# Optimization experiments

Measured on AMD Instinct MI355X. Metric: run time of the kernel, lower is better.

The kernel has to match this reference:

```python
import jax, jax.numpy as jnp
import numpy as np

B, T, C = 2, 2048, 2048
N_HEAD, D_HEAD = 16, 128

def setup_inputs() -> dict:
    key = jax.random.key(0)
    k1, k2, k3 = jax.random.split(key, 3)
    x = jax.random.normal(k1, (B, T, C), dtype=jnp.float32)
    # lecun-normal-ish scaling for kernels
    W_attn = jax.random.normal(k2, (C, 3 * C), dtype=jnp.float32) * (1.0 / np.sqrt(C))
    W_proj = jax.random.normal(k3, (C, C), dtype=jnp.float32) * (1.0 / np.sqrt(C))
    return {"x": x, "W_attn": W_attn, "W_proj": W_proj}

def reference(x, W_attn, W_proj):
    Bx, Tx, Cx = x.shape
    # fused qkv projection: (B,T,C) @ (C,3C)
    qkv = x @ W_attn
    q, k, v = jnp.split(qkv, 3, axis=-1)
    # (B, H, T, Dh)
    q = q.reshape(Bx, Tx, N_HEAD, D_HEAD).transpose(0, 2, 1, 3)
    k = k.reshape(Bx, Tx, N_HEAD, D_HEAD).transpose(0, 2, 1, 3)
    v = v.reshape(Bx, Tx, N_HEAD, D_HEAD).transpose(0, 2, 1, 3)
    scale = 1.0 / jnp.sqrt(jnp.asarray(D_HEAD, dtype=x.dtype))
    att = jnp.einsum('bhqd,bhkd->bhqk', q, k) * scale  # (B,H,T,T)
    causal_mask = jnp.tril(jnp.ones((Tx, Tx), dtype=jnp.bool_))[None, None]
    att = jnp.where(causal_mask, att, -jnp.inf)
    att = jax.nn.softmax(att, axis=-1)
    y = jnp.einsum('bhqk,bhkd->bhqd', att, v)
    y = y.transpose(0, 2, 1, 3).reshape(Bx, Tx, Cx)
    return y @ W_proj
```

## Files before the change

### kernel.cpp

```cpp
#include <hip/hip_runtime.h>
#include <hip/hip_bf16.h>
#include <stdint.h>

#define AS1 __attribute__((address_space(1)))
#define AS3 __attribute__((address_space(3)))

typedef __bf16 bf16_t;
typedef __bf16 bf16x8 __attribute__((ext_vector_type(8)));
typedef float f32x4 __attribute__((ext_vector_type(4)));
typedef float f32x16 __attribute__((ext_vector_type(16)));

static constexpr int Bsz = 2, T = 2048, Cdim = 2048, NH = 16, DH = 128;
static constexpr int M  = Bsz * T;
static constexpr int N1 = 3 * Cdim;
static constexpr int K1 = Cdim;

__device__ __forceinline__ unsigned short f2bf(float f) {
  unsigned u = __float_as_uint(f);
  u += 0x7fffu + ((u >> 16) & 1u);
  return (unsigned short)(u >> 16);
}

__device__ __forceinline__ void gload_lds16(const bf16_t* g, void* l) {
  __builtin_amdgcn_global_load_lds((AS1 const void*)g, (AS3 void*)l, 16, 0, 0);
}

__device__ __forceinline__ float ex2(float x) {
  float r; asm("v_exp_f32 %0, %1" : "=v"(r) : "v"(x)); return r;
}
__device__ __forceinline__ unsigned pk2(float a, float b) {
  unsigned r; asm("v_cvt_pk_bf16_f32 %0, %1, %2" : "=v"(r) : "v"(a), "v"(b)); return r;
}

__global__ __launch_bounds__(256) void preamble_kernel(const float* __restrict__ x,
                                                       const float* __restrict__ Wa,
                                                       const float* __restrict__ Wp,
                                                       unsigned short* __restrict__ xb,
                                                       unsigned short* __restrict__ WaT,
                                                       unsigned short* __restrict__ WpT) {
  __shared__ float tile[32][33];
  const int blk = blockIdx.x;
  const int tid = threadIdx.x;
  if (blk < 8192) {
    int i = blk * 1024 + tid * 4;
    float4 v = *(const float4*)(x + i);
    ushort4 o;
    o.x = f2bf(v.x); o.y = f2bf(v.y); o.z = f2bf(v.z); o.w = f2bf(v.w);
    *(ushort4*)(xb + i) = o;
    return;
  }
  const float* in;
  unsigned short* out;
  int Nn, bi;
  if (blk < 20480) { in = Wa; out = WaT; Nn = N1;   bi = blk - 8192;  }
  else             { in = Wp; out = WpT; Nn = Cdim; bi = blk - 20480; }
  const int ntiles = Nn >> 5;
  const int n0 = (bi % ntiles) * 32, k0 = (bi / ntiles) * 32;
  const int tx = tid & 31, ty = tid >> 5;
#pragma unroll
  for (int i = 0; i < 32; i += 8)
    tile[ty + i][tx] = in[(size_t)(k0 + ty + i) * Nn + n0 + tx];
  __syncthreads();
#pragma unroll
  for (int i = 0; i < 32; i += 8)
    out[(size_t)(n0 + ty + i) * K1 + k0 + tx] = f2bf(tile[tx][ty + i]);
}

template <int MODE>
__global__ __launch_bounds__(512, 4) void gemm_p3(const bf16_t* __restrict__ A,
                                                  const bf16_t* __restrict__ BT,
                                                  void* __restrict__ Cp,
                                                  int Nn, int Kk) {
  constexpr int SLOT = 24576;
  __shared__ __align__(16) char ldsmem[3 * SLOT];
  char* ldsb = ldsmem;

  const int tid = threadIdx.x;
  const int wid = tid >> 6, lane = tid & 63;
  const int lq = lane & 15, lk = lane >> 4;
  const int wr = wid >> 2, wc = wid & 3;

  const int bid = blockIdx.x;
  const int xcd = bid & 7;
  const int j = bid >> 3;
  const int r = j & 31, s5 = j >> 5;
  const int tn = s5 * 8 + (r & 7);
  const int tm = xcd * 4 + (r >> 3);

  f32x4 acc[4][4] = {};

  int aoff[4], boff[4];
#pragma unroll
  for (int m = 0; m < 4; ++m) {
    int row = wr * 64 + m * 16 + lq;
    aoff[m] = row * 64 + ((lk * 16) ^ (((row >> 1) & 3) << 4));
  }
#pragma unroll
  for (int n = 0; n < 4; ++n) {
    int brow = wc * 64 + n * 16 + lq;
    boff[n] = 8192 + brow * 64 + ((lk * 16) ^ (((brow >> 1) & 3) << 4));
  }

  const int pA = wid * 1024 + lane * 16;
  const int arow = pA >> 6;
  const int acsw = (pA & 63) ^ (((arow >> 1) & 3) << 4);
  const bf16_t* Ags = A + (size_t)(tm * 128 + arow) * Kk + (acsw >> 1);

  const int pB0 = wid * 1024 + lane * 16;
  const int brow0 = pB0 >> 6;
  const int bcsw0 = (pB0 & 63) ^ (((brow0 >> 1) & 3) << 4);
  const bf16_t* Bgs0 = BT + (size_t)(tn * 256 + brow0) * Kk + (bcsw0 >> 1);

  const int pB1 = 8192 + wid * 1024 + lane * 16;
  const int brow1 = pB1 >> 6;
  const int bcsw1 = (pB1 & 63) ^ (((brow1 >> 1) & 3) << 4);
  const bf16_t* Bgs1 = BT + (size_t)(tn * 256 + brow1) * Kk + (bcsw1 >> 1);

  const int ldsA = wid * 1024;
  const int ldsB0 = 8192 + wid * 1024;
  const int ldsB1 = 16384 + wid * 1024;

  auto stage = [&](int kt, int slot) {
    char* db = ldsb + slot * SLOT;
    gload_lds16(Ags + (size_t)kt * 32, db + ldsA);
    gload_lds16(Bgs0 + (size_t)kt * 32, db + ldsB0);
    gload_lds16(Bgs1 + (size_t)kt * 32, db + ldsB1);
  };

  const int nk = Kk >> 5;

  stage(0, 0); stage(1, 1);
  asm volatile("s_waitcnt vmcnt(3)" ::: "memory");
  __builtin_amdgcn_s_barrier();

#define TILE_BODY(KT, SLOT0, SLOT2, STAGE_EN, VM)                                \
  {                                                                              \
    __builtin_amdgcn_sched_barrier(0);                                           \
    const char* sb = ldsb + (SLOT0) * SLOT;                                      \
    bf16x8 af[4], bfv[4];                                                        \
    _Pragma("unroll") for (int m = 0; m < 4; ++m)                                \
      af[m] = *(const bf16x8*)(sb + aoff[m]);                                    \
    _Pragma("unroll") for (int n = 0; n < 4; ++n)                                \
      bfv[n] = *(const bf16x8*)(sb + boff[n]);                                   \
    if (STAGE_EN) stage((KT) + 2, (SLOT2));                                      \
    __builtin_amdgcn_sched_barrier(0);                                           \
    __builtin_amdgcn_s_barrier();                                                \
    asm volatile("s_waitcnt lgkmcnt(0)" ::: "memory");                           \
    __builtin_amdgcn_sched_barrier(0);                                           \
    __builtin_amdgcn_s_setprio(1);                                               \
    _Pragma("unroll") for (int m = 0; m < 4; ++m)                                \
      _Pragma("unroll") for (int n = 0; n < 4; ++n)                              \
        acc[m][n] =                                                              \
            __builtin_amdgcn_mfma_f32_16x16x32_bf16(af[m], bfv[n], acc[m][n], 0, 0, 0); \
    __builtin_amdgcn_s_setprio(0);                                               \
    __builtin_amdgcn_sched_barrier(0);                                           \
    asm volatile("s_waitcnt vmcnt(" #VM ")" ::: "memory");                       \
    __builtin_amdgcn_s_barrier();                                                \
  }

  {
    int c0 = 0;
    for (int kt = 0; kt < nk - 2; ++kt) {
      const int c2 = (c0 >= 1) ? (c0 - 1) : (c0 + 2);
      TILE_BODY(kt, c0, c2, 1, 3);
      c0 = (c0 >= 2) ? 0 : (c0 + 1);
    }
    TILE_BODY(nk - 2, c0, 0, 0, 0);
    c0 = (c0 >= 2) ? 0 : (c0 + 1);
    TILE_BODY(nk - 1, c0, 0, 0, 0);
  }
#undef TILE_BODY

  if (MODE == 1 && tn >= 16) {
    unsigned short* q16 = (unsigned short*)Cp;
#pragma unroll
    for (int m = 0; m < 4; ++m)
#pragma unroll
      for (int n = 0; n < 4; ++n) {
        int row = tm * 128 + wr * 64 + m * 16 + lk * 4;
        int b_ = row >> 11, t0 = row & 2047;
        int c = tn * 256 - 4096 + wc * 64 + n * 16 + lq;
        ushort4 o;
        o.x = f2bf(acc[m][n][0]); o.y = f2bf(acc[m][n][1]);
        o.z = f2bf(acc[m][n][2]); o.w = f2bf(acc[m][n][3]);
        *(ushort4*)(q16 + (size_t)(b_ * 2048 + c) * N1 + 4096 + t0) = o;
      }
  } else {
#pragma unroll
    for (int m = 0; m < 4; ++m)
#pragma unroll
      for (int n = 0; n < 4; ++n)
#pragma unroll
        for (int r2 = 0; r2 < 4; ++r2) {
          int row = tm * 128 + wr * 64 + m * 16 + lk * 4 + r2;
          int col = tn * 256 + wc * 64 + n * 16 + lq;
          if (MODE == 1)
            ((unsigned short*)Cp)[(size_t)row * Nn + col] = f2bf(acc[m][n][r2]);
          else
            ((float*)Cp)[(size_t)row * Nn + col] = acc[m][n][r2];
        }
  }
}

__global__ __launch_bounds__(512, 1) void attn_kernel(const bf16_t* __restrict__ qkv,
                                                      unsigned short* __restrict__ y) {
  __shared__ __align__(16) char lds[98304];
  const int tid = threadIdx.x;
  const int wid = tid >> 6, lane = tid & 63;
  const int l31 = lane & 31, hi = lane >> 5;
  const int hi16 = hi << 4;
  const int bh = blockIdx.x;
  const int g = blockIdx.y;
  const int b = bh >> 4, h = bh & 15;
  const float SC2 = 0.12751879868954096f;

  const int grp = (wid < 4) ? g : (15 - g);
  const int qlo = grp * 128 + (wid & 3) * 32;
  const int qidx = qlo + l31;
  const int nt = 2 * (15 - g) + 2;
  const size_t rowbase = (size_t)(b * T) * N1;

  bf16x8 qf[8];
  {
    const bf16_t* Qg = qkv + rowbase + (size_t)qidx * N1 + h * DH + hi * 8;
#pragma unroll
    for (int kk = 0; kk < 8; ++kk) qf[kk] = *(const bf16x8*)(Qg + kk * 16);
  }

  const bf16_t* Kg0 = qkv + rowbase + Cdim + h * DH;
  const bf16_t* Vg0 = qkv + (size_t)(b * 2048 + h * DH) * N1 + 2 * Cdim;
  const int p0 = wid * 1024 + lane * 16;
  const int p1 = 8192 + wid * 1024 + lane * 16;
  const int kr0 = p0 >> 8, kr1 = p1 >> 8;
  const bf16_t* KsA = Kg0 + (size_t)kr0 * N1 + ((((p0 & 255) ^ ((kr0 & 15) << 4))) >> 1);
  const bf16_t* KsB = Kg0 + (size_t)kr1 * N1 + ((((p1 & 255) ^ ((kr1 & 15) << 4))) >> 1);
  const int vr0 = p0 >> 7, vr1 = p1 >> 7;
  const bf16_t* VsA = Vg0 + (size_t)vr0 * N1 + ((((p0 & 127) ^ ((vr0 & 7) << 4))) >> 1);
  const bf16_t* VsB = Vg0 + (size_t)vr1 * N1 + ((((p1 & 127) ^ ((vr1 & 7) << 4))) >> 1);
  const int dstoff = wid * 1024;

  auto stage = [&](int tt, int slot) {
    char* Kd = lds + slot * 32768;
    char* Vd = Kd + 16384;
    const size_t ko = (size_t)(tt * 64) * N1;
    const int vo = tt * 64;
    gload_lds16(KsA + ko, Kd + dstoff);
    gload_lds16(KsB + ko, Kd + 8192 + dstoff);
    gload_lds16(VsA + vo, Vd + dstoff);
    gload_lds16(VsB + vo, Vd + 8192 + dstoff);
  };

  f32x16 oacc[4] = {};
  float mrow = -1e30f, lrow = 0.f;

  stage(0, 0); stage(1, 1);
  asm volatile("s_waitcnt vmcnt(4)" ::: "memory");
  __builtin_amdgcn_s_barrier();

  int cs = 0;
  for (int t = 0; t < nt; ++t) {
    const int kv0 = t * 64;
    if (t + 2 < nt) {
      const int s2 = (cs >= 1) ? (cs - 1) : (cs + 2);
      stage(t + 2, s2);
    }

    if (kv0 <= qlo + 31) {
      f32x16 s0 = {}, s1 = {};
      {
        const char* Kb = lds + cs * 32768;
        const char* krow0 = Kb + l31 * 256;
        const char* krow1 = Kb + (32 + l31) * 256;
        const int sw0 = (l31 & 15) << 4;
#pragma unroll
        for (int kk = 0; kk < 8; ++kk) {
          bf16x8 kf0 = *(const bf16x8*)(krow0 + ((kk * 32 + hi16) ^ sw0));
          bf16x8 kf1 = *(const bf16x8*)(krow1 + ((kk * 32 + hi16) ^ sw0));
          s0 = __builtin_amdgcn_mfma_f32_32x32x16_bf16(kf0, qf[kk], s0, 0, 0, 0);
          s1 = __builtin_amdgcn_mfma_f32_32x32x16_bf16(kf1, qf[kk], s1, 0, 0, 0);
        }
      }
      float sv[32];
#pragma unroll
      for (int r = 0; r < 16; ++r) { sv[r] = s0[r]; sv[16 + r] = s1[r]; }
      if (kv0 + 63 > qlo) {
#pragma unroll
        for (int r = 0; r < 16; ++r) {
          const int roff = (r & 3) + 8 * (r >> 2);
          if (kv0 + roff + 4 * hi > qidx) sv[r] = -1e30f;
          if (kv0 + 32 + roff + 4 * hi > qidx) sv[16 + r] = -1e30f;
        }
      }
      float mx = sv[0];
#pragma unroll
      for (int i = 1; i < 32; ++i) mx = fmaxf(mx, sv[i]);
      mx = fmaxf(mx, __shfl_xor(mx, 32));
      const float mn = fmaxf(mrow, mx);
      const float osc = ex2((mrow - mn) * SC2);
      mrow = mn;
      const float mn2 = mn * SC2;
#pragma unroll
      for (int db = 0; db < 4; ++db) oacc[db] *= osc;
      float srow = 0.f;
#pragma unroll
      for (int i = 0; i < 32; ++i) {
        float p = ex2(fmaf(sv[i], SC2, -mn2));
        sv[i] = p;
        srow += p;
      }
      srow += __shfl_xor(srow, 32);
      lrow = lrow * osc + srow;
      bf16x8 pb[4];
#pragma unroll
      for (int s4 = 0; s4 < 4; ++s4) {
        const int base = (s4 >> 1) * 16 + (s4 & 1) * 8;
        unsigned x0 = pk2(sv[base + 0], sv[base + 1]);
        unsigned x1 = pk2(sv[base + 2], sv[base + 3]);
        unsigned y0 = pk2(sv[base + 4], sv[base + 5]);
        unsigned y1 = pk2(sv[base + 6], sv[base + 7]);
        unsigned e0 = (unsigned)__shfl_xor((int)(hi ? x0 : y0), 32);
        unsigned e1 = (unsigned)__shfl_xor((int)(hi ? x1 : y1), 32);
        union { unsigned u[4]; bf16x8 v; } pbu;
        pbu.u[0] = hi ? e0 : x0;
        pbu.u[1] = hi ? e1 : x1;
        pbu.u[2] = hi ? y0 : e0;
        pbu.u[3] = hi ? y1 : e1;
        pb[s4] = pbu.v;
      }
      {
        const char* Vb = lds + cs * 32768 + 16384;
#pragma unroll
        for (int db = 0; db < 4; ++db) {
          const int vrow = db * 32 + l31;
          const char* vr = Vb + vrow * 128;
          const int swv = (vrow & 7) << 4;
#pragma unroll
          for (int s4 = 0; s4 < 4; ++s4) {
            bf16x8 vf = *(const bf16x8*)(vr + ((s4 * 32 + hi16) ^ swv));
            oacc[db] = __builtin_amdgcn_mfma_f32_32x32x16_bf16(vf, pb[s4], oacc[db], 0, 0, 0);
          }
        }
      }
    }

    asm volatile("s_waitcnt vmcnt(4)" ::: "memory");
    __builtin_amdgcn_s_barrier();
    cs = (cs >= 2) ? 0 : (cs + 1);
  }

  const float inv = 1.0f / lrow;
  char* eb = lds + wid * 8192;
#pragma unroll
  for (int db = 0; db < 4; ++db)
#pragma unroll
    for (int r = 0; r < 16; ++r) {
      const int d = db * 32 + (r & 3) + 8 * (r >> 2) + 4 * hi;
      const int off = l31 * 256 + ((d * 2) ^ ((l31 & 15) << 4));
      *(unsigned short*)(eb + off) = f2bf(oacc[db][r] * inv);
    }
  asm volatile("s_waitcnt lgkmcnt(0)" ::: "memory");
  __builtin_amdgcn_sched_barrier(0);
  {
    unsigned short* yr = y + (size_t)(b * T + qlo + l31) * Cdim + h * DH;
#pragma unroll
    for (int rr = 0; rr < 8; ++rr) {
      const int c = hi * 8 + rr;
      bf16x8 v = *(const bf16x8*)(eb + l31 * 256 + ((c * 16) ^ ((l31 & 15) << 4)));
      *(bf16x8*)(yr + c * 8) = v;
    }
  }
}

extern "C" void kernel_launch(void* const* d_in, const int* in_sizes, int n_in,
                              void* d_out, int out_size, void* d_ws, size_t ws_size,
                              hipStream_t stream) {
  const float* x  = (const float*)d_in[0];
  const float* Wa = (const float*)d_in[1];
  const float* Wp = (const float*)d_in[2];
  float* out = (float*)d_out;
  char* ws = (char*)d_ws;

  size_t o0 = 0;
  size_t o1 = o0 + (size_t)M * K1 * 2;
  size_t o2 = o1 + (size_t)N1 * K1 * 2;
  size_t o3 = o2 + (size_t)M * N1 * 2;
  size_t o4 = o3 + (size_t)M * Cdim * 2;

  unsigned short* xb   = (unsigned short*)(ws + o0);
  unsigned short* WaT  = (unsigned short*)(ws + o1);
  unsigned short* qkvb = (unsigned short*)(ws + o2);
  unsigned short* yb   = (unsigned short*)(ws + o3);
  unsigned short* WpT  = (unsigned short*)(ws + o4);

  preamble_kernel<<<dim3(24576), dim3(256), 0, stream>>>(x, Wa, Wp, xb, WaT, WpT);

  gemm_p3<1><<<dim3((M / 128) * (N1 / 256)), dim3(512), 0, stream>>>(
      (const bf16_t*)xb, (const bf16_t*)WaT, (void*)qkvb, N1, K1);

  attn_kernel<<<dim3(Bsz * NH, 8), dim3(512), 0, stream>>>(
      (const bf16_t*)qkvb, yb);

  gemm_p3<0><<<dim3((M / 128) * (Cdim / 256)), dim3(512), 0, stream>>>(
      (const bf16_t*)yb, (const bf16_t*)WpT, (void*)out, Cdim, K1);
}
```

Before: 232.9 us.

## Use 256x256-tile double-buffered GEMM with 8-phase schedule for QKV projection

```diff
diff --git a/kernel.cpp b/kernel.cpp
--- a/kernel.cpp
+++ b/kernel.cpp
@@ -64,6 +64,156 @@
 #pragma unroll
   for (int i = 0; i < 32; i += 8)
     out[(size_t)(n0 + ty + i) * K1 + k0 + tx] = f2bf(tile[tx][ty + i]);
+}
+
+template <int MODE>
+__global__ __launch_bounds__(512, 1) void gemm8p(const bf16_t* __restrict__ A,
+                                                 const bf16_t* __restrict__ BT,
+                                                 void* __restrict__ Cp,
+                                                 int Nn, int Kk) {
+  __shared__ __align__(16) char ldsmem[131072];
+  char* ldsb = ldsmem;
+  const char* sb0 = ldsmem;
+  const char* sb1 = ldsmem + 65536;
+
+  const int tid = threadIdx.x;
+  const int lane = tid & 63;
+  const int wid = tid >> 6;
+  const int lq = lane & 15, lk = lane >> 4;
+  const int wr = wid >> 2, wc = wid & 3;
+
+  const int bid = blockIdx.x;
+  const int xcd = bid & 7;
+  const int j = bid >> 3;
+  const int r = j & 15, s5 = j >> 4;
+  const int tn = s5 * 8 + (r & 7);
+  const int tm = xcd * 2 + (r >> 3);
+
+  f32x4 acc[8][4] = {};
+  bf16x8 afA[8], bf01[4], bf23[4];
+
+  const int r0 = tid >> 3;
+  const int c0 = (tid * 16) & 127;
+  const int csw = (c0 ^ ((r0 & 7) << 4)) >> 1;
+  const bf16_t* Agp = A + (size_t)(tm * 256 + r0) * Kk + csw;
+  const bf16_t* Bgp = BT + (size_t)(tn * 256 + r0) * Kk + csw;
+
+  auto stA = [&](int h, int kt, int d) {
+    char* db = ldsb + d * 65536 + h * 16384 + tid * 16;
+    const bf16_t* s = Agp + (size_t)(h * 128) * Kk + (size_t)kt * 64;
+    gload_lds16(s, db);
+    gload_lds16(s + (size_t)64 * Kk, db + 8192);
+  };
+  auto stB = [&](int h, int kt, int d) {
+    char* db = ldsb + 32768 + d * 65536 + h * 16384 + tid * 16;
+    const bf16_t* s = Bgp + (size_t)(h * 128) * Kk + (size_t)kt * 64;
+    gload_lds16(s, db);
+    gload_lds16(s + (size_t)64 * Kk, db + 8192);
+  };
+
+  auto rdA = [&](const char* sb, int h) {
+#pragma unroll
+    for (int m = 0; m < 4; ++m) {
+      const int rA = wr * 128 + (h * 4 + m) * 16 + lq;
+      const int sw = (rA & 7) << 4;
+      const char* rp = sb + rA * 128;
+      afA[m * 2 + 0] = *(const bf16x8*)(rp + ((lk * 16) ^ sw));
+      afA[m * 2 + 1] = *(const bf16x8*)(rp + ((64 + lk * 16) ^ sw));
+    }
+  };
+  auto rdB = [&](const char* sb, int nh, bf16x8* bfr) {
+#pragma unroll
+    for (int n = 0; n < 2; ++n) {
+      const int rB = wc * 64 + (nh * 2 + n) * 16 + lq;
+      const int sw = (rB & 7) << 4;
+      const char* rp = sb + 32768 + rB * 128;
+      bfr[n * 2 + 0] = *(const bf16x8*)(rp + ((lk * 16) ^ sw));
+      bfr[n * 2 + 1] = *(const bf16x8*)(rp + ((64 + lk * 16) ^ sw));
+    }
+  };
+  auto mmq = [&](const bf16x8* bfr, int mh, int nh) {
+#pragma unroll
+    for (int m = 0; m < 4; ++m)
+#pragma unroll
+      for (int n = 0; n < 2; ++n)
+#pragma unroll
+        for (int ks = 0; ks < 2; ++ks)
+          acc[mh * 4 + m][nh * 2 + n] = __builtin_amdgcn_mfma_f32_16x16x32_bf16(
+              afA[m * 2 + ks], bfr[n * 2 + ks], acc[mh * 4 + m][nh * 2 + n], 0, 0, 0);
+  };
+
+#define PH8(RD, ST, MH, NH, BF, VMSTR)                          \
+  {                                                             \
+    __builtin_amdgcn_sched_barrier(0);                          \
+    RD;                                                         \
+    ST;                                                         \
+    __builtin_amdgcn_sched_barrier(0);                          \
+    __builtin_amdgcn_s_barrier();                               \
+    asm volatile("s_waitcnt lgkmcnt(0)" ::: "memory");          \
+    __builtin_amdgcn_sched_barrier(0);                          \
+    __builtin_amdgcn_s_setprio(1);                              \
+    mmq(BF, MH, NH);                                            \
+    __builtin_amdgcn_s_setprio(0);                              \
+    __builtin_amdgcn_sched_barrier(0);                          \
+    asm volatile(VMSTR ::: "memory");                           \
+    __builtin_amdgcn_s_barrier();                               \
+  }
+
+#define ITER8(T1, T2, T3, STEN, VM3, VM7)                                        \
+  PH8((rdA(sb0, 0), rdB(sb0, 0, bf01)), stA(0, (T1), 1), 0, 0, bf01, "")         \
+  PH8(rdB(sb0, 1, bf23),                stA(1, (T1), 1), 0, 1, bf23, "")         \
+  PH8(rdA(sb0, 1),                      if (STEN) stB(0, (T2), 0), 1, 0, bf01, "") \
+  PH8((void)0,                          if (STEN) stB(1, (T2), 0), 1, 1, bf23, VM3) \
+  PH8((rdA(sb1, 0), rdB(sb1, 0, bf01)), if (STEN) stA(0, (T2), 0), 0, 0, bf01, "") \
+  PH8(rdB(sb1, 1, bf23),                if (STEN) stA(1, (T2), 0), 0, 1, bf23, "") \
+  PH8(rdA(sb1, 1),                      if (STEN) stB(0, (T3), 1), 1, 0, bf01, "") \
+  PH8((void)0,                          if (STEN) stB(1, (T3), 1), 1, 1, bf23, VM7)
+
+  stB(0, 0, 0); stB(1, 0, 0); stA(0, 0, 0); stA(1, 0, 0);
+  stB(0, 1, 1); stB(1, 1, 1);
+  asm volatile("s_waitcnt vmcnt(4)" ::: "memory");
+  __builtin_amdgcn_s_barrier();
+
+  for (int i = 0; i < 15; ++i) {
+    const int t1 = 2 * i + 1, t2 = 2 * i + 2, t3 = 2 * i + 3;
+    ITER8(t1, t2, t3, 1, "s_waitcnt vmcnt(4)", "s_waitcnt vmcnt(4)")
+  }
+  {
+    const int t1 = 31, t2 = 0, t3 = 0;
+    ITER8(t1, t2, t3, 0, "s_waitcnt vmcnt(0)", "")
+  }
+#undef ITER8
+#undef PH8
+
+  if (MODE == 1 && tn >= 16) {
+    unsigned short* q16 = (unsigned short*)Cp;
+#pragma unroll
+    for (int m = 0; m < 8; ++m)
+#pragma unroll
+      for (int n = 0; n < 4; ++n) {
+        int row = tm * 256 + wr * 128 + m * 16 + lk * 4;
+        int b_ = row >> 11, t0 = row & 2047;
+        int c = tn * 256 - 4096 + wc * 64 + n * 16 + lq;
+        ushort4 o;
+        o.x = f2bf(acc[m][n][0]); o.y = f2bf(acc[m][n][1]);
+        o.z = f2bf(acc[m][n][2]); o.w = f2bf(acc[m][n][3]);
+        *(ushort4*)(q16 + (size_t)(b_ * 2048 + c) * N1 + 4096 + t0) = o;
+      }
+  } else {
+#pragma unroll
+    for (int m = 0; m < 8; ++m)
+#pragma unroll
+      for (int n = 0; n < 4; ++n)
+#pragma unroll
+        for (int r2 = 0; r2 < 4; ++r2) {
+          int row = tm * 256 + wr * 128 + m * 16 + lk * 4 + r2;
+          int col = tn * 256 + wc * 64 + n * 16 + lq;
+          if (MODE == 1)
+            ((unsigned short*)Cp)[(size_t)row * Nn + col] = f2bf(acc[m][n][r2]);
+          else
+            ((float*)Cp)[(size_t)row * Nn + col] = acc[m][n][r2];
+        }
+  }
 }
 
 template <int MODE>
@@ -171,35 +321,19 @@
   }
 #undef TILE_BODY
 
-  if (MODE == 1 && tn >= 16) {
-    unsigned short* q16 = (unsigned short*)Cp;
-#pragma unroll
-    for (int m = 0; m < 4; ++m)
-#pragma unroll
-      for (int n = 0; n < 4; ++n) {
-        int row = tm * 128 + wr * 64 + m * 16 + lk * 4;
-        int b_ = row >> 11, t0 = row & 2047;
-        int c = tn * 256 - 4096 + wc * 64 + n * 16 + lq;
-        ushort4 o;
-        o.x = f2bf(acc[m][n][0]); o.y = f2bf(acc[m][n][1]);
-        o.z = f2bf(acc[m][n][2]); o.w = f2bf(acc[m][n][3]);
-        *(ushort4*)(q16 + (size_t)(b_ * 2048 + c) * N1 + 4096 + t0) = o;
-      }
-  } else {
-#pragma unroll
-    for (int m = 0; m < 4; ++m)
-#pragma unroll
-      for (int n = 0; n < 4; ++n)
-#pragma unroll
-        for (int r2 = 0; r2 < 4; ++r2) {
-          int row = tm * 128 + wr * 64 + m * 16 + lk * 4 + r2;
-          int col = tn * 256 + wc * 64 + n * 16 + lq;
-          if (MODE == 1)
-            ((unsigned short*)Cp)[(size_t)row * Nn + col] = f2bf(acc[m][n][r2]);
-          else
-            ((float*)Cp)[(size_t)row * Nn + col] = acc[m][n][r2];
-        }
-  }
+#pragma unroll
+  for (int m = 0; m < 4; ++m)
+#pragma unroll
+    for (int n = 0; n < 4; ++n)
+#pragma unroll
+      for (int r2 = 0; r2 < 4; ++r2) {
+        int row = tm * 128 + wr * 64 + m * 16 + lk * 4 + r2;
+        int col = tn * 256 + wc * 64 + n * 16 + lq;
+        if (MODE == 1)
+          ((unsigned short*)Cp)[(size_t)row * Nn + col] = f2bf(acc[m][n][r2]);
+        else
+          ((float*)Cp)[(size_t)row * Nn + col] = acc[m][n][r2];
+      }
 }
 
 __global__ __launch_bounds__(512, 1) void attn_kernel(const bf16_t* __restrict__ qkv,
@@ -394,7 +528,7 @@
 
   preamble_kernel<<<dim3(24576), dim3(256), 0, stream>>>(x, Wa, Wp, xb, WaT, WpT);
 
-  gemm_p3<1><<<dim3((M / 128) * (N1 / 256)), dim3(512), 0, stream>>>(
+  gemm8p<1><<<dim3((M / 256) * (N1 / 256)), dim3(512), 0, stream>>>(
       (const bf16_t*)xb, (const bf16_t*)WaT, (void*)qkvb, N1, K1);
 
   attn_kernel<<<dim3(Bsz * NH, 8), dim3(512), 0, stream>>>(
```

Result: slower. 245.1 us (+5.2%).
